# Kernel optimization log

Measured on AMD Instinct MI355X. Metric: run time of the kernel, lower is better.

The kernel has to match this reference:

```python
import jax, jax.numpy as jnp
import numpy as np

N = 8192
E = 262144
IN_DIM, HID_DIM, Z_DIM = 512, 256, 64


def setup_inputs() -> dict:
    key = jax.random.key(0)
    ks = jax.random.split(key, 8)
    x = jax.random.normal(ks[0], (N, IN_DIM), dtype=jnp.float32)
    edge_src = jax.random.randint(ks[1], (E,), 0, N, dtype=jnp.int32)
    edge_dst = jax.random.randint(ks[2], (E,), 0, N, dtype=jnp.int32)
    edge_w = jax.random.uniform(ks[3], (E,), dtype=jnp.float32)
    eps = jax.random.normal(ks[4], (N, Z_DIM), dtype=jnp.float32)
    # xavier-uniform linear weights (stored [in, out]); biases zero (as in torch init)
    def xavier(k, fan_in, fan_out):
        lim = float(np.sqrt(6.0 / (fan_in + fan_out)))
        return jax.random.uniform(k, (fan_in, fan_out), minval=-lim, maxval=lim, dtype=jnp.float32)
    W1 = xavier(ks[5], IN_DIM, HID_DIM)
    b1 = jnp.zeros((HID_DIM,), dtype=jnp.float32)
    Wmu = xavier(ks[6], HID_DIM, Z_DIM)
    bmu = jnp.zeros((Z_DIM,), dtype=jnp.float32)
    Wls = xavier(ks[7], HID_DIM, Z_DIM)
    bls = jnp.zeros((Z_DIM,), dtype=jnp.float32)
    return {"x": x, "edge_src": edge_src, "edge_dst": edge_dst, "edge_w": edge_w,
            "eps": eps, "W1": W1, "b1": b1, "Wmu": Wmu, "bmu": bmu, "Wls": Wls, "bls": bls}


def _spmm(edge_src, edge_dst, edge_w, h):
    # out[i] = sum_{(i,j) in edges} w_ij * h[j]  == torch.spmm(adj, h)
    return jax.ops.segment_sum(edge_w[:, None] * h[edge_dst], edge_src, num_segments=N)


def reference(x, edge_src, edge_dst, edge_w, eps, W1, b1, Wmu, bmu, Wls, bls):
    # GCN layer 1: linear -> spmm -> tanh
    h = jnp.tanh(_spmm(edge_src, edge_dst, edge_w, x @ W1 + b1))
    # mu / logstd heads (no activation)
    mu = _spmm(edge_src, edge_dst, edge_w, h @ Wmu + bmu)
    logstd = _spmm(edge_src, edge_dst, edge_w, h @ Wls + bls)
    # reparameterize (training mode): z = mu + eps * exp(logstd)
    z = mu + eps * jnp.exp(logstd)
    # inner-product decoder
    adj_logits = z @ z.T  # [N, N]
    return (z, adj_logits, mu, logstd)
```

## Files before the change

kernel.cpp:

```cpp
#include <hip/hip_runtime.h>
#include <math.h>

#define IN_DIM 512
#define HID    256
#define ZD     64

typedef short bf16x8 __attribute__((ext_vector_type(8)));
typedef float f32x4  __attribute__((ext_vector_type(4)));

__device__ inline unsigned short f2bf_rne(float f) {
    unsigned int b = __float_as_uint(f);
    b += 0x7FFFu + ((b >> 16) & 1u);
    return (unsigned short)(b >> 16);
}
__device__ inline float bf2f(unsigned short h) {
    return __uint_as_float(((unsigned int)h) << 16);
}


__global__ void k_zero_int(int* p, int n) {
    int i = blockIdx.x * blockDim.x + threadIdx.x;
    if (i < n) p[i] = 0;
}

__global__ void k_count(const int* __restrict__ src, int* __restrict__ deg, int E) {
    int e = blockIdx.x * blockDim.x + threadIdx.x;
    if (e < E) atomicAdd(&deg[src[e]], 1);
}

__global__ __launch_bounds__(256) void k_scan(const int* __restrict__ deg,
                                              int* __restrict__ rp,
                                              int* __restrict__ nxt, int N) {
    __shared__ int sums[256];
    int t = threadIdx.x;
    int chunk = N / 256;
    int base = t * chunk;
    int run = 0;
    for (int i = 0; i < chunk; ++i) run += deg[base + i];
    sums[t] = run;
    __syncthreads();
    for (int off = 1; off < 256; off <<= 1) {
        int u = (t >= off) ? sums[t - off] : 0;
        __syncthreads();
        sums[t] += u;
        __syncthreads();
    }
    int excl = (t == 0) ? 0 : sums[t - 1];
    int run2 = excl;
    for (int i = 0; i < chunk; ++i) {
        rp[base + i]  = run2;
        nxt[base + i] = run2;
        run2 += deg[base + i];
    }
    if (t == 255) rp[N] = run2;
}

__global__ void k_scatter(const int* __restrict__ src, const int* __restrict__ dst,
                          const float* __restrict__ w, int* __restrict__ nxt,
                          int* __restrict__ col, float* __restrict__ wv, int E) {
    int e = blockIdx.x * blockDim.x + threadIdx.x;
    if (e < E) {
        int pos = atomicAdd(&nxt[src[e]], 1);
        col[pos] = dst[e];
        wv[pos]  = w[e];
    }
}

__global__ void k_split_x(const float* __restrict__ x,
                          unsigned short* __restrict__ xh,
                          unsigned short* __restrict__ xl, int n4) {
    int i = blockIdx.x * blockDim.x + threadIdx.x;
    if (i < n4) {
        float4 v = *(const float4*)&x[(size_t)i * 4];
        float vv[4] = {v.x, v.y, v.z, v.w};
        ushort4 ho, lo;
        unsigned short* hp = (unsigned short*)&ho;
        unsigned short* lp = (unsigned short*)&lo;
        #pragma unroll
        for (int j = 0; j < 4; ++j) {
            unsigned short hcur = f2bf_rne(vv[j]);
            hp[j] = hcur;
            lp[j] = f2bf_rne(vv[j] - bf2f(hcur));
        }
        *(ushort4*)&xh[(size_t)i * 4] = ho;
        *(ushort4*)&xl[(size_t)i * 4] = lo;
    }
}

__global__ __launch_bounds__(256) void k_trans_w(const float* __restrict__ W,
                                                 unsigned short* __restrict__ Wt_h,
                                                 unsigned short* __restrict__ Wt_l,
                                                 int K, int Nw) {
    __shared__ float tile[32][33];
    int n0 = blockIdx.x * 32, k0 = blockIdx.y * 32;
    int tx = threadIdx.x, ty = threadIdx.y;
    #pragma unroll
    for (int j = 0; j < 4; ++j) {
        int k = ty + j * 8;
        tile[k][tx] = W[(size_t)(k0 + k) * Nw + n0 + tx];
    }
    __syncthreads();
    #pragma unroll
    for (int j = 0; j < 4; ++j) {
        int n = ty + j * 8;
        float v = tile[tx][n];
        size_t o = (size_t)(n0 + n) * K + k0 + tx;
        unsigned short hcur = f2bf_rne(v);
        Wt_h[o] = hcur;
        Wt_l[o] = f2bf_rne(v - bf2f(hcur));
    }
}

__global__ __launch_bounds__(256) void k_gemm1_mfma(const unsigned short* __restrict__ xh,
                                                    const unsigned short* __restrict__ xl,
                                                    const unsigned short* __restrict__ wth,
                                                    const unsigned short* __restrict__ wtl,
                                                    const float* __restrict__ b1,
                                                    float* __restrict__ h0) {
    int lane = threadIdx.x & 63;
    int w    = threadIdx.x >> 6;
    int rowBase = blockIdx.y * 64 + (w >> 1) * 32;
    int colBase = blockIdx.x * 64 + (w & 1) * 32;
    int m    = lane & 15;
    int quad = lane >> 4;
    int kofs = quad * 8;

    f32x4 acc[2][2] = {};
    #pragma unroll 2
    for (int k0 = 0; k0 < IN_DIM; k0 += 32) {
        bf16x8 xhf[2], xlf[2], whf[2], wlf[2];
        #pragma unroll
        for (int g = 0; g < 2; ++g) {
            size_t xoff = (size_t)(rowBase + g * 16 + m) * IN_DIM + k0 + kofs;
            xhf[g] = *(const bf16x8*)&xh[xoff];
            xlf[g] = *(const bf16x8*)&xl[xoff];
            size_t woff = (size_t)(colBase + g * 16 + m) * IN_DIM + k0 + kofs;
            whf[g] = *(const bf16x8*)&wth[woff];
            wlf[g] = *(const bf16x8*)&wtl[woff];
        }
        #pragma unroll
        for (int xg = 0; xg < 2; ++xg)
            #pragma unroll
            for (int wg = 0; wg < 2; ++wg) {
                acc[xg][wg] = __builtin_amdgcn_mfma_f32_16x16x32_bf16(whf[wg], xhf[xg], acc[xg][wg], 0, 0, 0);
                acc[xg][wg] = __builtin_amdgcn_mfma_f32_16x16x32_bf16(whf[wg], xlf[xg], acc[xg][wg], 0, 0, 0);
                acc[xg][wg] = __builtin_amdgcn_mfma_f32_16x16x32_bf16(wlf[wg], xhf[xg], acc[xg][wg], 0, 0, 0);
            }
    }
    #pragma unroll
    for (int wg = 0; wg < 2; ++wg) {
        float4 bv = *(const float4*)&b1[colBase + wg * 16 + quad * 4];
        float bb[4] = {bv.x, bv.y, bv.z, bv.w};
        #pragma unroll
        for (int xg = 0; xg < 2; ++xg) {
            f32x4 o = acc[xg][wg];
            #pragma unroll
            for (int r = 0; r < 4; ++r) o[r] += bb[r];
            *(f32x4*)&h0[(size_t)(rowBase + xg * 16 + m) * HID + colBase + wg * 16 + quad * 4] = o;
        }
    }
}

__global__ __launch_bounds__(256) void k_spmm_tanh(const int* __restrict__ rp,
                                                   const int* __restrict__ col,
                                                   const float* __restrict__ wv,
                                                   const float* __restrict__ h0,
                                                   float* __restrict__ h) {
    __shared__ int scol[256];
    __shared__ float sw[256];
    int i = blockIdx.x, t = threadIdx.x;
    int s = rp[i], e = rp[i + 1];
    float acc = 0.f;
    for (int cs = s; cs < e; cs += 256) {
        int n = min(256, e - cs);
        __syncthreads();
        if (t < n) { scol[t] = col[cs + t]; sw[t] = wv[cs + t]; }
        __syncthreads();
        #pragma unroll 4
        for (int p = 0; p < n; ++p)
            acc += sw[p] * h0[(size_t)scol[p] * HID + t];
    }
    h[(size_t)i * HID + t] = tanhf(acc);
}

__global__ __launch_bounds__(256) void k_heads(const float* __restrict__ h,
                                               const float* __restrict__ Wmu,
                                               const float* __restrict__ bmu,
                                               const float* __restrict__ Wls,
                                               const float* __restrict__ bls,
                                               float* __restrict__ hh) {
    __shared__ float ht[16][HID + 4];
    int t = threadIdx.x;
    int rowBase = blockIdx.x * 16;
    #pragma unroll
    for (int p = 0; p < 16; ++p)
        ht[p][t] = h[(size_t)(rowBase + p) * HID + t];
    __syncthreads();
    int c = t & 63, rg = t >> 6;
    float amu[4] = {}, als[4] = {};
    for (int k = 0; k < HID; k += 4) {
        float hv[4][4];
        #pragma unroll
        for (int r = 0; r < 4; ++r) {
            float4 tmp = *(const float4*)&ht[rg * 4 + r][k];
            hv[r][0] = tmp.x; hv[r][1] = tmp.y; hv[r][2] = tmp.z; hv[r][3] = tmp.w;
        }
        #pragma unroll
        for (int j = 0; j < 4; ++j) {
            float wm = Wmu[(k + j) * ZD + c];
            float wl = Wls[(k + j) * ZD + c];
            #pragma unroll
            for (int r = 0; r < 4; ++r) {
                amu[r] += hv[r][j] * wm;
                als[r] += hv[r][j] * wl;
            }
        }
    }
    float bm = bmu[c], bl = bls[c];
    #pragma unroll
    for (int r = 0; r < 4; ++r) {
        int row = rowBase + rg * 4 + r;
        hh[(size_t)row * 128 + c]      = amu[r] + bm;
        hh[(size_t)row * 128 + 64 + c] = als[r] + bl;
    }
}

__global__ __launch_bounds__(128) void k_spmm_heads(const int* __restrict__ rp,
                                                    const int* __restrict__ col,
                                                    const float* __restrict__ wv,
                                                    const float* __restrict__ hh,
                                                    const float* __restrict__ eps,
                                                    float* __restrict__ mu,
                                                    float* __restrict__ ls,
                                                    float* __restrict__ z,
                                                    unsigned short* __restrict__ zb) {
    __shared__ int scol[128];
    __shared__ float sw[128];
    __shared__ float sls[64];
    int i = blockIdx.x, t = threadIdx.x;
    int s = rp[i], e = rp[i + 1];
    float acc = 0.f;
    for (int cs = s; cs < e; cs += 128) {
        int n = min(128, e - cs);
        __syncthreads();
        if (t < n) { scol[t] = col[cs + t]; sw[t] = wv[cs + t]; }
        __syncthreads();
        #pragma unroll 4
        for (int p = 0; p < n; ++p)
            acc += sw[p] * hh[(size_t)scol[p] * 128 + t];
    }
    if (t >= 64) { ls[(size_t)i * ZD + t - 64] = acc; sls[t - 64] = acc; }
    __syncthreads();
    if (t < 64) {
        size_t o = (size_t)i * ZD + t;
        mu[o] = acc;
        float zz = acc + eps[o] * expf(sls[t]);
        z[o] = zz;
        zb[o] = f2bf_rne(zz);
    }
}

__global__ __launch_bounds__(256) void k_zzt_mfma(const unsigned short* __restrict__ zb,
                                                  float* __restrict__ out, int N) {
    int lane = threadIdx.x & 63;
    int w    = threadIdx.x >> 6;
    int waveRow = blockIdx.y * 128 + (w >> 1) * 64;
    int waveCol = blockIdx.x * 128 + (w & 1) * 64;
    int m    = lane & 15;
    int quad = lane >> 4;
    int kofs = quad * 8;

    bf16x8 a[4][2], b[4][2];
    #pragma unroll
    for (int rg = 0; rg < 4; ++rg) {
        const unsigned short* pr = zb + (size_t)(waveRow + rg * 16 + m) * ZD + kofs;
        const unsigned short* pc = zb + (size_t)(waveCol + rg * 16 + m) * ZD + kofs;
        a[rg][0] = *(const bf16x8*)pr;
        a[rg][1] = *(const bf16x8*)(pr + 32);
        b[rg][0] = *(const bf16x8*)pc;
        b[rg][1] = *(const bf16x8*)(pc + 32);
    }

    f32x4 acc[4][4] = {};
    #pragma unroll
    for (int rg = 0; rg < 4; ++rg)
        #pragma unroll
        for (int cg = 0; cg < 4; ++cg) {
            acc[rg][cg] = __builtin_amdgcn_mfma_f32_16x16x32_bf16(b[cg][0], a[rg][0], acc[rg][cg], 0, 0, 0);
            acc[rg][cg] = __builtin_amdgcn_mfma_f32_16x16x32_bf16(b[cg][1], a[rg][1], acc[rg][cg], 0, 0, 0);
        }

    #pragma unroll
    for (int rg = 0; rg < 4; ++rg) {
        size_t rowOff = (size_t)(waveRow + rg * 16 + m) * N;
        #pragma unroll
        for (int cg = 0; cg < 4; ++cg) {
            f32x4* po = (f32x4*)&out[rowOff + waveCol + cg * 16 + quad * 4];
            __builtin_nontemporal_store(acc[rg][cg], po);
        }
    }
}


extern "C" void kernel_launch(void* const* d_in, const int* in_sizes, int n_in,
                              void* d_out, int out_size, void* d_ws, size_t ws_size,
                              hipStream_t stream) {
    const float* x    = (const float*)d_in[0];
    const int*   esrc = (const int*)d_in[1];
    const int*   edst = (const int*)d_in[2];
    const float* ew   = (const float*)d_in[3];
    const float* eps  = (const float*)d_in[4];
    const float* W1   = (const float*)d_in[5];
    const float* b1   = (const float*)d_in[6];
    const float* Wmu  = (const float*)d_in[7];
    const float* bmu  = (const float*)d_in[8];
    const float* Wls  = (const float*)d_in[9];
    const float* bls  = (const float*)d_in[10];
    int N = in_sizes[0] / IN_DIM;
    int E = in_sizes[1];

    char* base = (char*)d_ws;
    size_t o = 0;
    #define ALLOC(ptr, type, count) type* ptr = (type*)(base + o); o = (o + (size_t)(count) * sizeof(type) + 63) & ~(size_t)63;
    ALLOC(h0,  float, (size_t)N * HID)
    ALLOC(h,   float, (size_t)N * HID)
    ALLOC(hh,  float, (size_t)N * 128)
    ALLOC(rp,  int,   N + 1)
    ALLOC(deg, int,   N)
    ALLOC(nxt, int,   N)
    ALLOC(col, int,   E)
    ALLOC(wv,  float, E)
    ALLOC(zb,  unsigned short, (size_t)N * ZD)
    ALLOC(xh,  unsigned short, (size_t)N * IN_DIM)
    ALLOC(xl,  unsigned short, (size_t)N * IN_DIM)
    ALLOC(wth, unsigned short, (size_t)IN_DIM * HID)
    ALLOC(wtl, unsigned short, (size_t)IN_DIM * HID)
    #undef ALLOC

    float* out_z   = (float*)d_out;
    float* out_adj = out_z + (size_t)N * ZD;
    float* out_mu  = out_adj + (size_t)N * N;
    float* out_ls  = out_mu + (size_t)N * ZD;

    k_zero_int<<<(N + 255) / 256, 256, 0, stream>>>(deg, N);
    k_count<<<(E + 255) / 256, 256, 0, stream>>>(esrc, deg, E);
    k_scan<<<1, 256, 0, stream>>>(deg, rp, nxt, N);
    k_scatter<<<(E + 255) / 256, 256, 0, stream>>>(esrc, edst, ew, nxt, col, wv, E);

    int n4 = N * IN_DIM / 4;
    k_split_x<<<(n4 + 255) / 256, 256, 0, stream>>>(x, xh, xl, n4);
    k_trans_w<<<dim3(HID / 32, IN_DIM / 32), dim3(32, 8), 0, stream>>>(W1, wth, wtl, IN_DIM, HID);

    k_gemm1_mfma<<<dim3(HID / 64, N / 64), 256, 0, stream>>>(xh, xl, wth, wtl, b1, h0);

    k_spmm_tanh<<<N, 256, 0, stream>>>(rp, col, wv, h0, h);

    k_heads<<<N / 16, 256, 0, stream>>>(h, Wmu, bmu, Wls, bls, hh);

    k_spmm_heads<<<N, 128, 0, stream>>>(rp, col, wv, hh, eps, out_mu, out_ls, out_z, zb);

    dim3 g2(N / 128, N / 128);
    k_zzt_mfma<<<g2, 256, 0, stream>>>(zb, out_adj, N);
}
```

Measured before the change: 484.2 us.

## Fuse x bf16 split into GEMM1, MFMA heads GEMM, merge weight prep kernels

The separate x split kernel goes away: GEMM1 now reads fp32 x directly and splits it into bf16 hi/lo parts in registers, which avoids writing and rereading two N x 512 bf16 buffers. The scalar FP32 heads kernel is replaced by a split-bf16 MFMA kernel, using weights pre-transposed by a single prep kernel that also zeroes the degree array. In exchange, GEMM1 repeats the conversion arithmetic for each column block (four per row of x), and the extra work per load could lengthen the MFMA loop.

```diff
diff --git a/kernel.cpp b/kernel.cpp
--- a/kernel.cpp
+++ b/kernel.cpp
@@ -17,11 +17,6 @@
     return __uint_as_float(((unsigned int)h) << 16);
 }
 
-
-__global__ void k_zero_int(int* p, int n) {
-    int i = blockIdx.x * blockDim.x + threadIdx.x;
-    if (i < n) p[i] = 0;
-}
 
 __global__ void k_count(const int* __restrict__ src, int* __restrict__ deg, int E) {
     int e = blockIdx.x * blockDim.x + threadIdx.x;
@@ -66,53 +61,55 @@
     }
 }
 
-__global__ void k_split_x(const float* __restrict__ x,
-                          unsigned short* __restrict__ xh,
-                          unsigned short* __restrict__ xl, int n4) {
-    int i = blockIdx.x * blockDim.x + threadIdx.x;
-    if (i < n4) {
-        float4 v = *(const float4*)&x[(size_t)i * 4];
-        float vv[4] = {v.x, v.y, v.z, v.w};
-        ushort4 ho, lo;
-        unsigned short* hp = (unsigned short*)&ho;
-        unsigned short* lp = (unsigned short*)&lo;
-        #pragma unroll
-        for (int j = 0; j < 4; ++j) {
-            unsigned short hcur = f2bf_rne(vv[j]);
-            hp[j] = hcur;
-            lp[j] = f2bf_rne(vv[j] - bf2f(hcur));
-        }
-        *(ushort4*)&xh[(size_t)i * 4] = ho;
-        *(ushort4*)&xl[(size_t)i * 4] = lo;
-    }
-}
-
-__global__ __launch_bounds__(256) void k_trans_w(const float* __restrict__ W,
-                                                 unsigned short* __restrict__ Wt_h,
-                                                 unsigned short* __restrict__ Wt_l,
-                                                 int K, int Nw) {
+__global__ __launch_bounds__(256) void k_prep(const float* __restrict__ W1,
+                                              const float* __restrict__ Wmu,
+                                              const float* __restrict__ Wls,
+                                              unsigned short* __restrict__ w1h,
+                                              unsigned short* __restrict__ w1l,
+                                              unsigned short* __restrict__ w2h,
+                                              unsigned short* __restrict__ w2l,
+                                              int* __restrict__ deg, int N) {
+    int bid = blockIdx.x;
+    int tx = threadIdx.x, ty = threadIdx.y;
+    if (bid == 160) {
+        int t = ty * 32 + tx;
+        for (int j = t; j < N; j += 256) deg[j] = 0;
+        return;
+    }
+    const float* src;
+    unsigned short *dh, *dl;
+    int Nw, ldd, rowOff, k0, n0;
+    if (bid < 128) {
+        src = W1; dh = w1h; dl = w1l; Nw = 256; ldd = 512; rowOff = 0;
+        n0 = (bid & 7) * 32; k0 = (bid >> 3) * 32;
+    } else if (bid < 144) {
+        int b = bid - 128;
+        src = Wmu; dh = w2h; dl = w2l; Nw = 64; ldd = 256; rowOff = 0;
+        n0 = (b & 1) * 32; k0 = (b >> 1) * 32;
+    } else {
+        int b = bid - 144;
+        src = Wls; dh = w2h; dl = w2l; Nw = 64; ldd = 256; rowOff = 64;
+        n0 = (b & 1) * 32; k0 = (b >> 1) * 32;
+    }
     __shared__ float tile[32][33];
-    int n0 = blockIdx.x * 32, k0 = blockIdx.y * 32;
-    int tx = threadIdx.x, ty = threadIdx.y;
     #pragma unroll
     for (int j = 0; j < 4; ++j) {
         int k = ty + j * 8;
-        tile[k][tx] = W[(size_t)(k0 + k) * Nw + n0 + tx];
+        tile[k][tx] = src[(size_t)(k0 + k) * Nw + n0 + tx];
     }
     __syncthreads();
     #pragma unroll
     for (int j = 0; j < 4; ++j) {
         int n = ty + j * 8;
         float v = tile[tx][n];
-        size_t o = (size_t)(n0 + n) * K + k0 + tx;
-        unsigned short hcur = f2bf_rne(v);
-        Wt_h[o] = hcur;
-        Wt_l[o] = f2bf_rne(v - bf2f(hcur));
-    }
-}
-
-__global__ __launch_bounds__(256) void k_gemm1_mfma(const unsigned short* __restrict__ xh,
-                                                    const unsigned short* __restrict__ xl,
+        size_t o = (size_t)(rowOff + n0 + n) * ldd + k0 + tx;
+        unsigned short hc = f2bf_rne(v);
+        dh[o] = hc;
+        dl[o] = f2bf_rne(v - bf2f(hc));
+    }
+}
+
+__global__ __launch_bounds__(256) void k_gemm1_mfma(const float* __restrict__ x,
                                                     const unsigned short* __restrict__ wth,
                                                     const unsigned short* __restrict__ wtl,
                                                     const float* __restrict__ b1,
@@ -131,9 +128,20 @@
         bf16x8 xhf[2], xlf[2], whf[2], wlf[2];
         #pragma unroll
         for (int g = 0; g < 2; ++g) {
-            size_t xoff = (size_t)(rowBase + g * 16 + m) * IN_DIM + k0 + kofs;
-            xhf[g] = *(const bf16x8*)&xh[xoff];
-            xlf[g] = *(const bf16x8*)&xl[xoff];
+            const float* px = x + (size_t)(rowBase + g * 16 + m) * IN_DIM + k0 + kofs;
+            f32x4 v0 = *(const f32x4*)px;
+            f32x4 v1 = *(const f32x4*)(px + 4);
+            unsigned short* hp = (unsigned short*)&xhf[g];
+            unsigned short* lp = (unsigned short*)&xlf[g];
+            #pragma unroll
+            for (int j = 0; j < 4; ++j) {
+                unsigned short hc0 = f2bf_rne(v0[j]);
+                hp[j] = hc0;
+                lp[j] = f2bf_rne(v0[j] - bf2f(hc0));
+                unsigned short hc1 = f2bf_rne(v1[j]);
+                hp[4 + j] = hc1;
+                lp[4 + j] = f2bf_rne(v1[j] - bf2f(hc1));
+            }
             size_t woff = (size_t)(colBase + g * 16 + m) * IN_DIM + k0 + kofs;
             whf[g] = *(const bf16x8*)&wth[woff];
             wlf[g] = *(const bf16x8*)&wtl[woff];
@@ -183,45 +191,65 @@
     h[(size_t)i * HID + t] = tanhf(acc);
 }
 
-__global__ __launch_bounds__(256) void k_heads(const float* __restrict__ h,
-                                               const float* __restrict__ Wmu,
-                                               const float* __restrict__ bmu,
-                                               const float* __restrict__ Wls,
-                                               const float* __restrict__ bls,
-                                               float* __restrict__ hh) {
-    __shared__ float ht[16][HID + 4];
-    int t = threadIdx.x;
-    int rowBase = blockIdx.x * 16;
-    #pragma unroll
-    for (int p = 0; p < 16; ++p)
-        ht[p][t] = h[(size_t)(rowBase + p) * HID + t];
-    __syncthreads();
-    int c = t & 63, rg = t >> 6;
-    float amu[4] = {}, als[4] = {};
-    for (int k = 0; k < HID; k += 4) {
-        float hv[4][4];
-        #pragma unroll
-        for (int r = 0; r < 4; ++r) {
-            float4 tmp = *(const float4*)&ht[rg * 4 + r][k];
-            hv[r][0] = tmp.x; hv[r][1] = tmp.y; hv[r][2] = tmp.z; hv[r][3] = tmp.w;
-        }
-        #pragma unroll
-        for (int j = 0; j < 4; ++j) {
-            float wm = Wmu[(k + j) * ZD + c];
-            float wl = Wls[(k + j) * ZD + c];
-            #pragma unroll
-            for (int r = 0; r < 4; ++r) {
-                amu[r] += hv[r][j] * wm;
-                als[r] += hv[r][j] * wl;
+__global__ __launch_bounds__(256) void k_heads_mfma(const float* __restrict__ h,
+                                                    const unsigned short* __restrict__ w2h,
+                                                    const unsigned short* __restrict__ w2l,
+                                                    const float* __restrict__ bmu,
+                                                    const float* __restrict__ bls,
+                                                    float* __restrict__ hh) {
+    int lane = threadIdx.x & 63;
+    int w    = threadIdx.x >> 6;
+    int rowBase = blockIdx.y * 64 + (w >> 1) * 32;
+    int colBase = blockIdx.x * 64 + (w & 1) * 32;
+    int m    = lane & 15;
+    int quad = lane >> 4;
+    int kofs = quad * 8;
+
+    f32x4 acc[2][2] = {};
+    #pragma unroll 2
+    for (int k0 = 0; k0 < HID; k0 += 32) {
+        bf16x8 xhf[2], xlf[2], whf[2], wlf[2];
+        #pragma unroll
+        for (int g = 0; g < 2; ++g) {
+            const float* ph = h + (size_t)(rowBase + g * 16 + m) * HID + k0 + kofs;
+            f32x4 v0 = *(const f32x4*)ph;
+            f32x4 v1 = *(const f32x4*)(ph + 4);
+            unsigned short* hp = (unsigned short*)&xhf[g];
+            unsigned short* lp = (unsigned short*)&xlf[g];
+            #pragma unroll
+            for (int j = 0; j < 4; ++j) {
+                unsigned short hc0 = f2bf_rne(v0[j]);
+                hp[j] = hc0;
+                lp[j] = f2bf_rne(v0[j] - bf2f(hc0));
+                unsigned short hc1 = f2bf_rne(v1[j]);
+                hp[4 + j] = hc1;
+                lp[4 + j] = f2bf_rne(v1[j] - bf2f(hc1));
             }
-        }
-    }
-    float bm = bmu[c], bl = bls[c];
-    #pragma unroll
-    for (int r = 0; r < 4; ++r) {
-        int row = rowBase + rg * 4 + r;
-        hh[(size_t)row * 128 + c]      = amu[r] + bm;
-        hh[(size_t)row * 128 + 64 + c] = als[r] + bl;
+            size_t woff = (size_t)(colBase + g * 16 + m) * HID + k0 + kofs;
+            whf[g] = *(const bf16x8*)&w2h[woff];
+            wlf[g] = *(const bf16x8*)&w2l[woff];
+        }
+        #pragma unroll
+        for (int xg = 0; xg < 2; ++xg)
+            #pragma unroll
+            for (int wg = 0; wg < 2; ++wg) {
+                acc[xg][wg] = __builtin_amdgcn_mfma_f32_16x16x32_bf16(whf[wg], xhf[xg], acc[xg][wg], 0, 0, 0);
+                acc[xg][wg] = __builtin_amdgcn_mfma_f32_16x16x32_bf16(whf[wg], xlf[xg], acc[xg][wg], 0, 0, 0);
+                acc[xg][wg] = __builtin_amdgcn_mfma_f32_16x16x32_bf16(wlf[wg], xhf[xg], acc[xg][wg], 0, 0, 0);
+            }
+    }
+    #pragma unroll
+    for (int wg = 0; wg < 2; ++wg) {
+        int cg = colBase + wg * 16 + quad * 4;
+        float4 bv = (cg < 64) ? *(const float4*)&bmu[cg] : *(const float4*)&bls[cg - 64];
+        float bb[4] = {bv.x, bv.y, bv.z, bv.w};
+        #pragma unroll
+        for (int xg = 0; xg < 2; ++xg) {
+            f32x4 o = acc[xg][wg];
+            #pragma unroll
+            for (int r = 0; r < 4; ++r) o[r] += bb[r];
+            *(f32x4*)&hh[(size_t)(rowBase + xg * 16 + m) * 128 + cg] = o;
+        }
     }
 }
 
@@ -331,10 +359,10 @@
     ALLOC(col, int,   E)
     ALLOC(wv,  float, E)
     ALLOC(zb,  unsigned short, (size_t)N * ZD)
-    ALLOC(xh,  unsigned short, (size_t)N * IN_DIM)
-    ALLOC(xl,  unsigned short, (size_t)N * IN_DIM)
-    ALLOC(wth, unsigned short, (size_t)IN_DIM * HID)
-    ALLOC(wtl, unsigned short, (size_t)IN_DIM * HID)
+    ALLOC(w1h, unsigned short, (size_t)IN_DIM * HID)
+    ALLOC(w1l, unsigned short, (size_t)IN_DIM * HID)
+    ALLOC(w2h, unsigned short, (size_t)128 * HID)
+    ALLOC(w2l, unsigned short, (size_t)128 * HID)
     #undef ALLOC
 
     float* out_z   = (float*)d_out;
@@ -342,20 +370,17 @@
     float* out_mu  = out_adj + (size_t)N * N;
     float* out_ls  = out_mu + (size_t)N * ZD;
 
-    k_zero_int<<<(N + 255) / 256, 256, 0, stream>>>(deg, N);
+    k_prep<<<161, dim3(32, 8), 0, stream>>>(W1, Wmu, Wls, w1h, w1l, w2h, w2l, deg, N);
+
     k_count<<<(E + 255) / 256, 256, 0, stream>>>(esrc, deg, E);
     k_scan<<<1, 256, 0, stream>>>(deg, rp, nxt, N);
     k_scatter<<<(E + 255) / 256, 256, 0, stream>>>(esrc, edst, ew, nxt, col, wv, E);
 
-    int n4 = N * IN_DIM / 4;
-    k_split_x<<<(n4 + 255) / 256, 256, 0, stream>>>(x, xh, xl, n4);
-    k_trans_w<<<dim3(HID / 32, IN_DIM / 32), dim3(32, 8), 0, stream>>>(W1, wth, wtl, IN_DIM, HID);
-
-    k_gemm1_mfma<<<dim3(HID / 64, N / 64), 256, 0, stream>>>(xh, xl, wth, wtl, b1, h0);
+    k_gemm1_mfma<<<dim3(HID / 64, N / 64), 256, 0, stream>>>(x, w1h, w1l, b1, h0);
 
     k_spmm_tanh<<<N, 256, 0, stream>>>(rp, col, wv, h0, h);
 
-    k_heads<<<N / 16, 256, 0, stream>>>(h, Wmu, bmu, Wls, bls, hh);
+    k_heads_mfma<<<dim3(2, N / 64), 256, 0, stream>>>(h, w2h, w2l, bmu, bls, hh);
 
     k_spmm_heads<<<N, 128, 0, stream>>>(rp, col, wv, hh, eps, out_mu, out_ls, out_z, zb);
 
```

Result: faster. 462.8 us (-4.4%).
